# Kernel optimization log

Measured on AMD Instinct MI355X. Metric: run time of the kernel, lower is better.

Reference implementation:

```python
import jax, jax.numpy as jnp
import numpy as np

N = 100000        # nodes
E = 1600000       # edges
D = 128           # feature dim (all layers)
G = 128           # graphs
C = 10            # num_classes
L = 3             # conv layers
EPS = 1e-5
SLOPE = 0.03


def setup_inputs() -> dict:
    key = jax.random.key(0)
    ks = jax.random.split(key, 12)
    x = jax.random.normal(ks[0], (N, D), dtype=jnp.float32)
    edge_index = jax.random.randint(ks[1], (2, E), 0, N, dtype=jnp.int64)
    batch = jnp.sort(jax.random.randint(ks[2], (N,), 0, G, dtype=jnp.int64))
    s = 1.0 / np.sqrt(D)
    Wc = jax.random.uniform(ks[3], (L, D, D), jnp.float32, -s, s)
    bc = jax.random.uniform(ks[4], (L, D), jnp.float32, -s, s)
    bn_gamma = jnp.ones((2, D), jnp.float32)
    bn_beta = jnp.zeros((2, D), jnp.float32)
    bn_mean = jax.random.normal(ks[5], (2, D), jnp.float32) * 0.1
    bn_var = jax.random.uniform(ks[6], (2, D), jnp.float32, 0.5, 1.5)
    lin_w = jax.random.uniform(ks[7], (C, D), jnp.float32, -s, s)
    lin_b = jax.random.uniform(ks[8], (C,), jnp.float32, -s, s)
    return {"x": x, "edge_index": edge_index, "batch": batch, "Wc": Wc,
            "bc": bc, "bn_gamma": bn_gamma, "bn_beta": bn_beta,
            "bn_mean": bn_mean, "bn_var": bn_var, "lin_w": lin_w, "lin_b": lin_b}


def _gcn_norm(edge_index):
    # add self-loops, compute D^{-1/2}[row] * D^{-1/2}[col] (PyG gcn_norm)
    loops = jnp.arange(N, dtype=edge_index.dtype)
    row = jnp.concatenate([edge_index[0], loops])
    col = jnp.concatenate([edge_index[1], loops])
    deg = jax.ops.segment_sum(jnp.ones_like(col, dtype=jnp.float32), col, num_segments=N)
    dis = jnp.where(deg > 0, jax.lax.rsqrt(deg), 0.0)
    return row, col, dis[row] * dis[col]


def reference(x, edge_index, batch, Wc, bc, bn_gamma, bn_beta, bn_mean, bn_var, lin_w, lin_b):
    row, col, norm = _gcn_norm(edge_index)
    h = x
    for i in range(L):
        h = h @ Wc[i]                                          # linear transform [N, D]
        msg = h[row] * norm[:, None]                           # gather + normalize [E+N, D]
        h = jax.ops.segment_sum(msg, col, num_segments=N) + bc[i]
        if i < 2:  # batchnorm only for i < len(batchnorms)-1 (eval mode, running stats)
            h = (h - bn_mean[i]) * jax.lax.rsqrt(bn_var[i] + EPS) * bn_gamma[i] + bn_beta[i]
        h = jnp.where(h > 0, h, SLOPE * h)                     # LeakyReLU(0.03)
    # global mean pool over graphs
    counts = jax.ops.segment_sum(jnp.ones((N,), jnp.float32), batch, num_segments=G)
    pooled = jax.ops.segment_sum(h, batch, num_segments=G) / jnp.maximum(counts, 1.0)[:, None]
    # dropout is identity in eval; final linear head
    return pooled @ lin_w.T + lin_b                            # [G, C]
```

## Files before the change

kernel.cpp:

```cpp
#include <hip/hip_runtime.h>
#include <hip/hip_bf16.h>

#define NN 100000
#define EE 1600000
#define DD 128
#define GG 128
#define CC 10
#define NPB 256
#define NB 391
#define SCAP 5120
#define VPT 16
#define CPAD 32
#define PPN 64

typedef __attribute__((ext_vector_type(8))) short bf16x8;
typedef __attribute__((ext_vector_type(4))) float f32x4;
typedef __attribute__((ext_vector_type(2))) float f32x2;
typedef unsigned int u32;

__device__ inline float blo(u32 u) { return __uint_as_float(u << 16); }
__device__ inline float bhi(u32 u) { return __uint_as_float(u & 0xffff0000u); }
__device__ inline u32 bpack(float x, float y) {
    u32 bx = __float_as_uint(x);
    u32 by = __float_as_uint(y);
    bx = (bx + 0x7fffu + ((bx >> 16) & 1u)) >> 16;
    by = (by + 0x7fffu + ((by >> 16) & 1u)) & 0xffff0000u;
    return bx | by;
}

__global__ __launch_bounds__(256) void k_bcount(const int* __restrict__ col,
                                                int* __restrict__ bhist) {
    __shared__ int lh[NB];
    int tid = threadIdx.x;
    for (int b = tid; b < NB; b += 256) lh[b] = 0;
    __syncthreads();
    int base = blockIdx.x * (256 * VPT);
#pragma unroll
    for (int j = 0; j < VPT; j++) {
        int e = base + j * 256 + tid;
        if (e < EE) atomicAdd(&lh[col[e] >> 8], 1);
    }
    __syncthreads();
    for (int b = tid; b < NB; b += 256) {
        int h = lh[b];
        if (h) atomicAdd(&bhist[b * CPAD], h);
    }
}

__global__ __launch_bounds__(512) void k_bscan(const int* __restrict__ bhist,
                                               int* __restrict__ boffs,
                                               int* __restrict__ bcur) {
    __shared__ int s[512];
    int tid = threadIdx.x;
    int c = (tid < NB) ? bhist[tid * CPAD] : 0;
    s[tid] = c;
    __syncthreads();
    for (int off = 1; off < 512; off <<= 1) {
        int v = (tid >= off) ? s[tid - off] : 0;
        __syncthreads();
        s[tid] += v;
        __syncthreads();
    }
    int excl = s[tid] - c;
    if (tid < NB) {
        boffs[tid] = excl;
        bcur[tid * CPAD] = excl;
    }
    if (tid == NB - 1) boffs[NB] = excl + c;
}

__global__ __launch_bounds__(256) void k_part(const int* __restrict__ row, const int* __restrict__ col,
                                              int* __restrict__ bcur, u32* __restrict__ pairs) {
    __shared__ int lhist[NB];
    __shared__ int gbase[NB];
    __shared__ int lcur[NB];
    int tid = threadIdx.x;
    for (int b = tid; b < NB; b += 256) lhist[b] = 0;
    __syncthreads();
    int base = blockIdx.x * (256 * VPT);
    u32 v[VPT];
    int bb[VPT];
#pragma unroll
    for (int j = 0; j < VPT; j++) {
        int e = base + j * 256 + tid;
        if (e < EE) {
            int r = row[e], c = col[e];
            v[j] = ((u32)r << 8) | (u32)(c & 255);
            bb[j] = c >> 8;
            atomicAdd(&lhist[bb[j]], 1);
        } else {
            bb[j] = -1;
        }
    }
    __syncthreads();
    for (int b = tid; b < NB; b += 256) {
        int h = lhist[b];
        gbase[b] = h ? atomicAdd(&bcur[b * CPAD], h) : 0;
        lcur[b] = 0;
    }
    __syncthreads();
#pragma unroll
    for (int j = 0; j < VPT; j++) {
        if (bb[j] >= 0) {
            int slot = gbase[bb[j]] + atomicAdd(&lcur[bb[j]], 1);
            pairs[slot] = v[j];
        }
    }
}

__global__ __launch_bounds__(256) void k_sort(const u32* __restrict__ pairs,
                                              const int* __restrict__ boffs,
                                              int* __restrict__ offs,
                                              float* __restrict__ dis,
                                              int* __restrict__ src) {
    int b = blockIdx.x;
    int tid = threadIdx.x;
    int nstart = b << 8;
    int nvalid = NN - nstart;
    if (nvalid > NPB) nvalid = NPB;
    int base = boffs[b];
    int eend = boffs[b + 1];
    int cnt = eend - base;
    __shared__ int lcnt[NPB];
    __shared__ int lscan[NPB];
    __shared__ int lcur[NPB];
    __shared__ int lsrc[SCAP];
    lcnt[tid] = 0;
    __syncthreads();
    for (int e = base + tid; e < eend; e += 256)
        atomicAdd(&lcnt[pairs[e] & 255u], 1);
    __syncthreads();
    int c = lcnt[tid];
    lscan[tid] = c;
    __syncthreads();
    for (int off = 1; off < 256; off <<= 1) {
        int v = (tid >= off) ? lscan[tid - off] : 0;
        __syncthreads();
        lscan[tid] += v;
        __syncthreads();
    }
    int excl = lscan[tid] - c;
    if (tid < nvalid) {
        offs[nstart + tid] = base + excl;
        dis[nstart + tid] = rsqrtf((float)(c + 1));
    }
    if (b == NB - 1 && tid == 255) offs[NN] = EE;
    lcur[tid] = excl;
    __syncthreads();
    if (cnt <= SCAP) {
        for (int e = base + tid; e < eend; e += 256) {
            u32 v = pairs[e];
            int slot = atomicAdd(&lcur[v & 255u], 1);
            lsrc[slot] = (int)(v >> 8);
        }
        __syncthreads();
        for (int i = tid; i < cnt; i += 256)
            src[base + i] = lsrc[i];
    } else {
        for (int e = base + tid; e < eend; e += 256) {
            u32 v = pairs[e];
            int slot = base + atomicAdd(&lcur[v & 255u], 1);
            src[slot] = (int)(v >> 8);
        }
    }
}

__global__ void k_prep(const float* __restrict__ Wc, const float* __restrict__ bc,
                       const float* __restrict__ gamma, const float* __restrict__ beta,
                       const float* __restrict__ mean, const float* __restrict__ var,
                       __hip_bfloat16* __restrict__ WT,
                       float* __restrict__ tc) {
    int i = blockIdx.x * 256 + threadIdx.x;
    if (i < 3 * 128) {
        int l = i >> 7, d = i & 127;
        float t;
        if (l < 2) {
            float s = gamma[l * 128 + d] * rsqrtf(var[l * 128 + d] + 1e-5f);
            t = (bc[l * 128 + d] - mean[l * 128 + d]) * s + beta[l * 128 + d];
        } else {
            t = bc[2 * 128 + d];
        }
        tc[i] = t;
    }
    if (i < 3 * 16384) {
        int l = i >> 14, r = (i >> 7) & 127, k = i & 127;
        float s = 1.f;
        if (l < 2) s = gamma[l * 128 + r] * rsqrtf(var[l * 128 + r] + 1e-5f);
        WT[i] = __float2bfloat16(Wc[l * 16384 + k * 128 + r] * s);
    }
}

__global__ __launch_bounds__(256) void k_pre(const float* __restrict__ x,
                                             const float* __restrict__ dis,
                                             u32* __restrict__ hs) {
    int i = blockIdx.x * 256 + threadIdx.x;
    if (i < NN * 64) {
        float dn = dis[i >> 6];
        float2 v = ((const float2*)x)[i];
        hs[i] = bpack(v.x * dn, v.y * dn);
    }
}

template <int PRESCALE>
__global__ __launch_bounds__(1024) void k_aggT(const u32* __restrict__ hin,
                                               const int* __restrict__ offs,
                                               const int* __restrict__ src,
                                               const float* __restrict__ dis,
                                               const __hip_bfloat16* __restrict__ WT,
                                               const float* __restrict__ tc,
                                               u32* __restrict__ hout) {
    __shared__ u32   Atile[16][68];
    __shared__ float Otile[16][132];
    int wid = threadIdx.x >> 6;
    int lane = threadIdx.x & 63;
    int node = blockIdx.x * 16 + wid;
    int e0 = __builtin_amdgcn_readfirstlane(offs[node]);
    int e1 = __builtin_amdgcn_readfirstlane(offs[node + 1]);
    u32 self = hin[((u32)node << 6) + lane];
    f32x2 acc = {blo(self), bhi(self)};
    int e = e0;
    for (; e + 16 <= e1; e += 16) {
        u32 u[16];
#pragma unroll
        for (int j = 0; j < 16; j++) {
            u32 s = (u32)src[e + j];
            u[j] = hin[(s << 6) + lane];
        }
#pragma unroll
        for (int j = 0; j < 16; j++) {
            f32x2 v = {blo(u[j]), bhi(u[j])};
            acc += v;
        }
    }
    for (; e + 8 <= e1; e += 8) {
        u32 u[8];
#pragma unroll
        for (int j = 0; j < 8; j++) {
            u32 s = (u32)src[e + j];
            u[j] = hin[(s << 6) + lane];
        }
#pragma unroll
        for (int j = 0; j < 8; j++) {
            f32x2 v = {blo(u[j]), bhi(u[j])};
            acc += v;
        }
    }
    for (; e < e1; e++) {
        u32 u = hin[((u32)src[e] << 6) + lane];
        f32x2 v = {blo(u), bhi(u)};
        acc += v;
    }
    float dn = dis[node];
    Atile[wid][lane] = bpack(acc.x * dn, acc.y * dn);
    __syncthreads();
    if (wid < 8) {
        int lg = lane >> 4, lr = lane & 15;
        f32x4 c4 = {0.f, 0.f, 0.f, 0.f};
#pragma unroll
        for (int kk = 0; kk < 4; kk++) {
            bf16x8 a = *(const bf16x8*)&Atile[lr][kk * 16 + lg * 4];
            bf16x8 b = *(const bf16x8*)(WT + (size_t)(wid * 16 + lr) * 128 + kk * 32 + lg * 8);
            c4 = __builtin_amdgcn_mfma_f32_16x16x32_bf16(a, b, c4, 0, 0, 0);
        }
#pragma unroll
        for (int r = 0; r < 4; r++)
            Otile[lg * 4 + r][wid * 16 + lr] = c4[r];
    }
    __syncthreads();
    int d0 = lane * 2;
    float r0 = Otile[wid][d0]     + tc[d0];
    float r1 = Otile[wid][d0 + 1] + tc[d0 + 1];
    r0 = r0 > 0.f ? r0 : 0.03f * r0;
    r1 = r1 > 0.f ? r1 : 0.03f * r1;
    if (PRESCALE) { r0 *= dn; r1 *= dn; }
    hout[((u32)node << 6) + lane] = bpack(r0, r1);
}

__global__ __launch_bounds__(64) void k_pool(const u32* __restrict__ h,
                                             const int* __restrict__ batch,
                                             float* __restrict__ pooled,
                                             float* __restrict__ counts) {
    int lane = threadIdx.x;
    int n0 = blockIdx.x * PPN;
    if (n0 >= NN) return;
    int n1 = n0 + PPN;
    if (n1 > NN) n1 = NN;
    float a0 = 0.f, a1 = 0.f, cnt = 0.f;
    int g = batch[n0];
    for (int n = n0; n < n1; n++) {
        int bg = batch[n];
        if (bg != g) {
            atomicAdd(&pooled[g * 128 + lane * 2], a0);
            atomicAdd(&pooled[g * 128 + lane * 2 + 1], a1);
            if (lane == 0) atomicAdd(&counts[g], cnt);
            a0 = 0.f; a1 = 0.f; cnt = 0.f; g = bg;
        }
        u32 u = h[(u32)n * 64u + lane];
        a0 += blo(u); a1 += bhi(u);
        cnt += 1.f;
    }
    atomicAdd(&pooled[g * 128 + lane * 2], a0);
    atomicAdd(&pooled[g * 128 + lane * 2 + 1], a1);
    if (lane == 0) atomicAdd(&counts[g], cnt);
}

__global__ void k_head(const float* __restrict__ pooled, const float* __restrict__ counts,
                       const float* __restrict__ w, const float* __restrict__ b,
                       float* __restrict__ out) {
    int i = blockIdx.x * blockDim.x + threadIdx.x;
    if (i >= GG * CC) return;
    int g = i / CC, c = i % CC;
    float cnt = counts[g];
    cnt = cnt > 1.f ? cnt : 1.f;
    float inv = 1.f / cnt;
    const float* p = &pooled[g * 128];
    const float* ww = &w[c * 128];
    float acc = 0.f;
    for (int d = 0; d < 128; d++) acc += p[d] * ww[d];
    out[i] = acc * inv + b[c];
}

extern "C" void kernel_launch(void* const* d_in, const int* in_sizes, int n_in,
                              void* d_out, int out_size, void* d_ws, size_t ws_size,
                              hipStream_t stream) {
    const float* x     = (const float*)d_in[0];
    const int*   ei    = (const int*)d_in[1];
    const int*   row   = ei;
    const int*   col   = ei + EE;
    const int*   batch = (const int*)d_in[2];
    const float* Wc    = (const float*)d_in[3];
    const float* bc    = (const float*)d_in[4];
    const float* gamma = (const float*)d_in[5];
    const float* beta  = (const float*)d_in[6];
    const float* mean  = (const float*)d_in[7];
    const float* var   = (const float*)d_in[8];
    const float* lw    = (const float*)d_in[9];
    const float* lb    = (const float*)d_in[10];
    float* out = (float*)d_out;

    char* p = (char*)d_ws;
    auto alloc = [&](size_t bytes) -> char* {
        char* r = p;
        p += (bytes + 255) & ~(size_t)255;
        return r;
    };
    float* dis    = (float*)alloc((size_t)NN * 4);
    int*   offs   = (int*)alloc((size_t)(NN + 1) * 4);
    int*   bhist  = (int*)alloc((size_t)NB * CPAD * 4);
    int*   boffs  = (int*)alloc((size_t)(NB + 1) * 4);
    int*   bcur   = (int*)alloc((size_t)NB * CPAD * 4);
    int*   src    = (int*)alloc((size_t)EE * 4);
    __hip_bfloat16* WT = (__hip_bfloat16*)alloc((size_t)3 * 16384 * 2);
    float* tc     = (float*)alloc((size_t)3 * 128 * 4);
    float* pooled = (float*)alloc((size_t)GG * 128 * 4);
    float* counts = (float*)alloc((size_t)GG * 4);
    __hip_bfloat16* h0b = (__hip_bfloat16*)alloc((size_t)NN * 128 * 2);
    __hip_bfloat16* h1b = (__hip_bfloat16*)alloc((size_t)NN * 128 * 2);
    u32* pairs = (u32*)h0b;

    hipMemsetAsync(bhist, 0, (size_t)NB * CPAD * 4, stream);
    hipMemsetAsync(pooled, 0, (size_t)GG * 128 * 4, stream);
    hipMemsetAsync(counts, 0, (size_t)GG * 4, stream);

    const int eb_grid = (EE + 256 * VPT - 1) / (256 * VPT);
    k_bcount<<<eb_grid, 256, 0, stream>>>(col, bhist);
    k_bscan<<<1, 512, 0, stream>>>(bhist, boffs, bcur);
    k_part<<<eb_grid, 256, 0, stream>>>(row, col, bcur, pairs);
    k_sort<<<NB, 256, 0, stream>>>(pairs, boffs, offs, dis, src);
    k_prep<<<192, 256, 0, stream>>>(Wc, bc, gamma, beta, mean, var, WT, tc);
    k_pre<<<(NN * 64 + 255) / 256, 256, 0, stream>>>(x, dis, (u32*)h0b);

    const int fused_grid = NN / 16;

    k_aggT<1><<<fused_grid, 1024, 0, stream>>>((const u32*)h0b, offs, src, dis, WT,           tc,       (u32*)h1b);
    k_aggT<1><<<fused_grid, 1024, 0, stream>>>((const u32*)h1b, offs, src, dis, WT + 16384,   tc + 128, (u32*)h0b);
    k_aggT<0><<<fused_grid, 1024, 0, stream>>>((const u32*)h0b, offs, src, dis, WT + 2*16384, tc + 256, (u32*)h1b);

    k_pool<<<(NN + PPN - 1) / PPN, 64, 0, stream>>>((const u32*)h1b, batch, pooled, counts);
    k_head<<<(GG * CC + 255) / 256, 256, 0, stream>>>(pooled, counts, lw, lb, out);
}
```

Baseline: 379.9 us.

## Sort nodes by in-degree so each aggregation block handles similar-degree nodes

Adds a counting sort of nodes by in-degree (histogram, scan, fill kernels) that builds a permutation. Each wave of the fused aggregate+transform kernel then processes permuted nodes, so the 16 waves in a block have similar edge counts. The aim is to reduce load imbalance and idle waves that wait at block barriers. In exchange it adds three small kernels and an extra indirection, and it scatters output writes and self reads, which loses the locality of sequential node order.

```diff
diff --git a/kernel.cpp b/kernel.cpp
--- a/kernel.cpp
+++ b/kernel.cpp
@@ -12,6 +12,7 @@
 #define VPT 16
 #define CPAD 32
 #define PPN 64
+#define DB 256
 
 typedef __attribute__((ext_vector_type(8))) short bf16x8;
 typedef __attribute__((ext_vector_type(4))) float f32x4;
@@ -112,6 +113,7 @@
                                               const int* __restrict__ boffs,
                                               int* __restrict__ offs,
                                               float* __restrict__ dis,
+                                              int* __restrict__ deg,
                                               int* __restrict__ src) {
     int b = blockIdx.x;
     int tid = threadIdx.x;
@@ -143,6 +145,7 @@
     if (tid < nvalid) {
         offs[nstart + tid] = base + excl;
         dis[nstart + tid] = rsqrtf((float)(c + 1));
+        deg[nstart + tid] = c;
     }
     if (b == NB - 1 && tid == 255) offs[NN] = EE;
     lcur[tid] = excl;
@@ -161,6 +164,75 @@
             u32 v = pairs[e];
             int slot = base + atomicAdd(&lcur[v & 255u], 1);
             src[slot] = (int)(v >> 8);
+        }
+    }
+}
+
+__global__ __launch_bounds__(256) void k_dhist(const int* __restrict__ deg,
+                                               int* __restrict__ dh) {
+    __shared__ int lh[DB];
+    int tid = threadIdx.x;
+    lh[tid] = 0;
+    __syncthreads();
+    int base = blockIdx.x * 1024;
+#pragma unroll
+    for (int j = 0; j < 4; j++) {
+        int n = base + j * 256 + tid;
+        if (n < NN) {
+            int d = deg[n]; if (d > 255) d = 255;
+            atomicAdd(&lh[d], 1);
+        }
+    }
+    __syncthreads();
+    int h = lh[tid];
+    if (h) atomicAdd(&dh[tid * CPAD], h);
+}
+
+__global__ __launch_bounds__(256) void k_dscan(const int* __restrict__ dh,
+                                               int* __restrict__ dcur) {
+    __shared__ int s[DB];
+    int tid = threadIdx.x;
+    int c = dh[tid * CPAD];
+    s[tid] = c;
+    __syncthreads();
+    for (int off = 1; off < DB; off <<= 1) {
+        int v = (tid >= off) ? s[tid - off] : 0;
+        __syncthreads();
+        s[tid] += v;
+        __syncthreads();
+    }
+    dcur[tid * CPAD] = s[tid] - c;
+}
+
+__global__ __launch_bounds__(256) void k_dfill(const int* __restrict__ deg,
+                                               int* __restrict__ dcur,
+                                               int* __restrict__ perm) {
+    __shared__ int lh[DB];
+    __shared__ int gb[DB];
+    __shared__ int lc[DB];
+    int tid = threadIdx.x;
+    lh[tid] = 0;
+    __syncthreads();
+    int base = blockIdx.x * 1024;
+    int d[4];
+#pragma unroll
+    for (int j = 0; j < 4; j++) {
+        int n = base + j * 256 + tid;
+        if (n < NN) {
+            d[j] = deg[n]; if (d[j] > 255) d[j] = 255;
+            atomicAdd(&lh[d[j]], 1);
+        } else d[j] = -1;
+    }
+    __syncthreads();
+    int h = lh[tid];
+    gb[tid] = h ? atomicAdd(&dcur[tid * CPAD], h) : 0;
+    lc[tid] = 0;
+    __syncthreads();
+#pragma unroll
+    for (int j = 0; j < 4; j++) {
+        if (d[j] >= 0) {
+            int r = atomicAdd(&lc[d[j]], 1);
+            perm[gb[d[j]] + r] = base + j * 256 + tid;
         }
     }
 }
@@ -206,6 +278,7 @@
                                                const int* __restrict__ offs,
                                                const int* __restrict__ src,
                                                const float* __restrict__ dis,
+                                               const int* __restrict__ perm,
                                                const __hip_bfloat16* __restrict__ WT,
                                                const float* __restrict__ tc,
                                                u32* __restrict__ hout) {
@@ -213,7 +286,7 @@
     __shared__ float Otile[16][132];
     int wid = threadIdx.x >> 6;
     int lane = threadIdx.x & 63;
-    int node = blockIdx.x * 16 + wid;
+    int node = __builtin_amdgcn_readfirstlane(perm[blockIdx.x * 16 + wid]);
     int e0 = __builtin_amdgcn_readfirstlane(offs[node]);
     int e1 = __builtin_amdgcn_readfirstlane(offs[node + 1]);
     u32 self = hin[((u32)node << 6) + lane];
@@ -346,9 +419,13 @@
     };
     float* dis    = (float*)alloc((size_t)NN * 4);
     int*   offs   = (int*)alloc((size_t)(NN + 1) * 4);
+    int*   deg    = (int*)alloc((size_t)NN * 4);
+    int*   perm   = (int*)alloc((size_t)NN * 4);
     int*   bhist  = (int*)alloc((size_t)NB * CPAD * 4);
     int*   boffs  = (int*)alloc((size_t)(NB + 1) * 4);
     int*   bcur   = (int*)alloc((size_t)NB * CPAD * 4);
+    int*   dh     = (int*)alloc((size_t)DB * CPAD * 4);
+    int*   dcur   = (int*)alloc((size_t)DB * CPAD * 4);
     int*   src    = (int*)alloc((size_t)EE * 4);
     __hip_bfloat16* WT = (__hip_bfloat16*)alloc((size_t)3 * 16384 * 2);
     float* tc     = (float*)alloc((size_t)3 * 128 * 4);
@@ -359,22 +436,27 @@
     u32* pairs = (u32*)h0b;
 
     hipMemsetAsync(bhist, 0, (size_t)NB * CPAD * 4, stream);
+    hipMemsetAsync(dh, 0, (size_t)DB * CPAD * 4, stream);
     hipMemsetAsync(pooled, 0, (size_t)GG * 128 * 4, stream);
     hipMemsetAsync(counts, 0, (size_t)GG * 4, stream);
 
     const int eb_grid = (EE + 256 * VPT - 1) / (256 * VPT);
+    const int nd_grid = (NN + 1023) / 1024;
     k_bcount<<<eb_grid, 256, 0, stream>>>(col, bhist);
     k_bscan<<<1, 512, 0, stream>>>(bhist, boffs, bcur);
     k_part<<<eb_grid, 256, 0, stream>>>(row, col, bcur, pairs);
-    k_sort<<<NB, 256, 0, stream>>>(pairs, boffs, offs, dis, src);
+    k_sort<<<NB, 256, 0, stream>>>(pairs, boffs, offs, dis, deg, src);
+    k_dhist<<<nd_grid, 256, 0, stream>>>(deg, dh);
+    k_dscan<<<1, 256, 0, stream>>>(dh, dcur);
+    k_dfill<<<nd_grid, 256, 0, stream>>>(deg, dcur, perm);
     k_prep<<<192, 256, 0, stream>>>(Wc, bc, gamma, beta, mean, var, WT, tc);
     k_pre<<<(NN * 64 + 255) / 256, 256, 0, stream>>>(x, dis, (u32*)h0b);
 
     const int fused_grid = NN / 16;
 
-    k_aggT<1><<<fused_grid, 1024, 0, stream>>>((const u32*)h0b, offs, src, dis, WT,           tc,       (u32*)h1b);
-    k_aggT<1><<<fused_grid, 1024, 0, stream>>>((const u32*)h1b, offs, src, dis, WT + 16384,   tc + 128, (u32*)h0b);
-    k_aggT<0><<<fused_grid, 1024, 0, stream>>>((const u32*)h0b, offs, src, dis, WT + 2*16384, tc + 256, (u32*)h1b);
+    k_aggT<1><<<fused_grid, 1024, 0, stream>>>((const u32*)h0b, offs, src, dis, perm, WT,           tc,       (u32*)h1b);
+    k_aggT<1><<<fused_grid, 1024, 0, stream>>>((const u32*)h1b, offs, src, dis, perm, WT + 16384,   tc + 128, (u32*)h0b);
+    k_aggT<0><<<fused_grid, 1024, 0, stream>>>((const u32*)h0b, offs, src, dis, perm, WT + 2*16384, tc + 256, (u32*)h1b);
 
     k_pool<<<(NN + PPN - 1) / PPN, 64, 0, stream>>>((const u32*)h1b, batch, pooled, counts);
     k_head<<<(GG * CC + 255) / 256, 256, 0, stream>>>(pooled, counts, lw, lb, out);
```

Result: faster. 370.5 us (-2.5%).

## Split fused aggregate+transform kernel into separate gather and MFMA transform kernels

Applied to the files above, without the earlier changes.

Replaces the fused 1024-thread kernel, which did the neighbour gather and then an MFMA transform in one block, with two kernels per layer. A 256-thread gather kernel writes the aggregated bf16 rows to memory, and a separate 512-thread kernel applies the 128x128 MFMA transform, bias and LeakyReLU in place. The aim is to drop the block-wide syncs and large blocks that stall gather waves, and to let small blocks schedule flexibly for better latency hiding. The cost is an extra round trip of the node features through global memory and three extra launches.

```diff
diff --git a/kernel.cpp b/kernel.cpp
--- a/kernel.cpp
+++ b/kernel.cpp
@@ -201,19 +201,14 @@
     }
 }
 
-template <int PRESCALE>
-__global__ __launch_bounds__(1024) void k_aggT(const u32* __restrict__ hin,
-                                               const int* __restrict__ offs,
-                                               const int* __restrict__ src,
-                                               const float* __restrict__ dis,
-                                               const __hip_bfloat16* __restrict__ WT,
-                                               const float* __restrict__ tc,
-                                               u32* __restrict__ hout) {
-    __shared__ u32   Atile[16][68];
-    __shared__ float Otile[16][132];
-    int wid = threadIdx.x >> 6;
+__global__ __launch_bounds__(256) void k_agg2(const u32* __restrict__ hin,
+                                              const int* __restrict__ offs,
+                                              const int* __restrict__ src,
+                                              const float* __restrict__ dis,
+                                              u32* __restrict__ aggout) {
+    int node = (blockIdx.x << 2) + (threadIdx.x >> 6);
     int lane = threadIdx.x & 63;
-    int node = blockIdx.x * 16 + wid;
+    if (node >= NN) return;
     int e0 = __builtin_amdgcn_readfirstlane(offs[node]);
     int e1 = __builtin_amdgcn_readfirstlane(offs[node + 1]);
     u32 self = hin[((u32)node << 6) + lane];
@@ -251,29 +246,45 @@
         acc += v;
     }
     float dn = dis[node];
-    Atile[wid][lane] = bpack(acc.x * dn, acc.y * dn);
-    __syncthreads();
-    if (wid < 8) {
-        int lg = lane >> 4, lr = lane & 15;
-        f32x4 c4 = {0.f, 0.f, 0.f, 0.f};
-#pragma unroll
-        for (int kk = 0; kk < 4; kk++) {
-            bf16x8 a = *(const bf16x8*)&Atile[lr][kk * 16 + lg * 4];
-            bf16x8 b = *(const bf16x8*)(WT + (size_t)(wid * 16 + lr) * 128 + kk * 32 + lg * 8);
-            c4 = __builtin_amdgcn_mfma_f32_16x16x32_bf16(a, b, c4, 0, 0, 0);
-        }
-#pragma unroll
-        for (int r = 0; r < 4; r++)
-            Otile[lg * 4 + r][wid * 16 + lr] = c4[r];
-    }
-    __syncthreads();
-    int d0 = lane * 2;
-    float r0 = Otile[wid][d0]     + tc[d0];
-    float r1 = Otile[wid][d0 + 1] + tc[d0 + 1];
-    r0 = r0 > 0.f ? r0 : 0.03f * r0;
-    r1 = r1 > 0.f ? r1 : 0.03f * r1;
-    if (PRESCALE) { r0 *= dn; r1 *= dn; }
-    hout[((u32)node << 6) + lane] = bpack(r0, r1);
+    aggout[((u32)node << 6) + lane] = bpack(acc.x * dn, acc.y * dn);
+}
+
+template <int PRESCALE>
+__global__ __launch_bounds__(512) void k_trans(u32* __restrict__ h,
+                                               const float* __restrict__ dis,
+                                               const __hip_bfloat16* __restrict__ WT,
+                                               const float* __restrict__ tc) {
+    __shared__ u32   Atile[16][68];
+    __shared__ float Otile[16][132];
+    int tid = threadIdx.x;
+    int row0 = blockIdx.x * 16;
+    for (int i = tid; i < 1024; i += 512)
+        Atile[i >> 6][i & 63] = h[(u32)row0 * 64u + i];
+    __syncthreads();
+    int wid = tid >> 6, lane = tid & 63;
+    int lg = lane >> 4, lr = lane & 15;
+    f32x4 c4 = {0.f, 0.f, 0.f, 0.f};
+#pragma unroll
+    for (int kk = 0; kk < 4; kk++) {
+        bf16x8 a = *(const bf16x8*)&Atile[lr][kk * 16 + lg * 4];
+        bf16x8 b = *(const bf16x8*)(WT + (size_t)(wid * 16 + lr) * 128 + kk * 32 + lg * 8);
+        c4 = __builtin_amdgcn_mfma_f32_16x16x32_bf16(a, b, c4, 0, 0, 0);
+    }
+#pragma unroll
+    for (int r = 0; r < 4; r++)
+        Otile[lg * 4 + r][wid * 16 + lr] = c4[r];
+    __syncthreads();
+    for (int i = tid; i < 1024; i += 512) {
+        int rw = i >> 6, cp = i & 63;
+        int node = row0 + rw;
+        int d0 = cp * 2;
+        float r0 = Otile[rw][d0]     + tc[d0];
+        float r1 = Otile[rw][d0 + 1] + tc[d0 + 1];
+        r0 = r0 > 0.f ? r0 : 0.03f * r0;
+        r1 = r1 > 0.f ? r1 : 0.03f * r1;
+        if (PRESCALE) { float dn = dis[node]; r0 *= dn; r1 *= dn; }
+        h[(u32)node * 64u + cp] = bpack(r0, r1);
+    }
 }
 
 __global__ __launch_bounds__(64) void k_pool(const u32* __restrict__ h,
@@ -370,11 +381,15 @@
     k_prep<<<192, 256, 0, stream>>>(Wc, bc, gamma, beta, mean, var, WT, tc);
     k_pre<<<(NN * 64 + 255) / 256, 256, 0, stream>>>(x, dis, (u32*)h0b);
 
-    const int fused_grid = NN / 16;
-
-    k_aggT<1><<<fused_grid, 1024, 0, stream>>>((const u32*)h0b, offs, src, dis, WT,           tc,       (u32*)h1b);
-    k_aggT<1><<<fused_grid, 1024, 0, stream>>>((const u32*)h1b, offs, src, dis, WT + 16384,   tc + 128, (u32*)h0b);
-    k_aggT<0><<<fused_grid, 1024, 0, stream>>>((const u32*)h0b, offs, src, dis, WT + 2*16384, tc + 256, (u32*)h1b);
+    const int agg_grid   = NN / 4;
+    const int trans_grid = NN / 16;
+
+    k_agg2<<<agg_grid, 256, 0, stream>>>((const u32*)h0b, offs, src, dis, (u32*)h1b);
+    k_trans<1><<<trans_grid, 512, 0, stream>>>((u32*)h1b, dis, WT, tc);
+    k_agg2<<<agg_grid, 256, 0, stream>>>((const u32*)h1b, offs, src, dis, (u32*)h0b);
+    k_trans<1><<<trans_grid, 512, 0, stream>>>((u32*)h0b, dis, WT + 16384, tc + 128);
+    k_agg2<<<agg_grid, 256, 0, stream>>>((const u32*)h0b, offs, src, dis, (u32*)h1b);
+    k_trans<0><<<trans_grid, 512, 0, stream>>>((u32*)h1b, dis, WT + 2 * 16384, tc + 256);
 
     k_pool<<<(NN + PPN - 1) / PPN, 64, 0, stream>>>((const u32*)h1b, batch, pooled, counts);
     k_head<<<(GG * CC + 255) / 256, 256, 0, stream>>>(pooled, counts, lw, lb, out);
```

After: 387.9 us. 1.02x slower.

## Make each wave aggregate eight nodes and run its own MFMA transform

Applied to the files above, without the earlier changes.

The fused aggregate-plus-transform kernel now has each 64-lane wave gather eight nodes serially, then compute all eight output column tiles with MFMA from its own LDS tile. This removes the block-wide __syncthreads barriers and the idle waves in the old layout, where 16 waves each handled one node and only 8 of them ran MFMA. In exchange, each wave's gather latency is serialized across its eight nodes. Half of each MFMA's A rows are duplicates and are wasted, and blocks shrink to 256 threads.

```diff
diff --git a/kernel.cpp b/kernel.cpp
--- a/kernel.cpp
+++ b/kernel.cpp
@@ -202,78 +202,89 @@
 }
 
 template <int PRESCALE>
-__global__ __launch_bounds__(1024) void k_aggT(const u32* __restrict__ hin,
-                                               const int* __restrict__ offs,
-                                               const int* __restrict__ src,
-                                               const float* __restrict__ dis,
-                                               const __hip_bfloat16* __restrict__ WT,
-                                               const float* __restrict__ tc,
-                                               u32* __restrict__ hout) {
-    __shared__ u32   Atile[16][68];
-    __shared__ float Otile[16][132];
-    int wid = threadIdx.x >> 6;
-    int lane = threadIdx.x & 63;
-    int node = blockIdx.x * 16 + wid;
-    int e0 = __builtin_amdgcn_readfirstlane(offs[node]);
-    int e1 = __builtin_amdgcn_readfirstlane(offs[node + 1]);
-    u32 self = hin[((u32)node << 6) + lane];
-    f32x2 acc = {blo(self), bhi(self)};
-    int e = e0;
-    for (; e + 16 <= e1; e += 16) {
-        u32 u[16];
-#pragma unroll
-        for (int j = 0; j < 16; j++) {
-            u32 s = (u32)src[e + j];
-            u[j] = hin[(s << 6) + lane];
-        }
-#pragma unroll
-        for (int j = 0; j < 16; j++) {
-            f32x2 v = {blo(u[j]), bhi(u[j])};
+__global__ __launch_bounds__(256) void k_aggW(const u32* __restrict__ hin,
+                                              const int* __restrict__ offs,
+                                              const int* __restrict__ src,
+                                              const float* __restrict__ dis,
+                                              const __hip_bfloat16* __restrict__ WT,
+                                              const float* __restrict__ tc,
+                                              u32* __restrict__ hout) {
+    __shared__ u32   Atile[4][8][68];
+    __shared__ float Otile[4][8][132];
+    int tid = threadIdx.x;
+    int w = tid >> 6, lane = tid & 63;
+    int base = blockIdx.x * 32 + w * 8;
+    float dns[8];
+#pragma unroll
+    for (int i = 0; i < 8; i++) {
+        int node = base + i;
+        int e0 = __builtin_amdgcn_readfirstlane(offs[node]);
+        int e1 = __builtin_amdgcn_readfirstlane(offs[node + 1]);
+        u32 self = hin[((u32)node << 6) + lane];
+        f32x2 acc = {blo(self), bhi(self)};
+        int e = e0;
+        for (; e + 16 <= e1; e += 16) {
+            u32 u[16];
+#pragma unroll
+            for (int j = 0; j < 16; j++) {
+                u32 s = (u32)src[e + j];
+                u[j] = hin[(s << 6) + lane];
+            }
+#pragma unroll
+            for (int j = 0; j < 16; j++) {
+                f32x2 v = {blo(u[j]), bhi(u[j])};
+                acc += v;
+            }
+        }
+        for (; e + 8 <= e1; e += 8) {
+            u32 u[8];
+#pragma unroll
+            for (int j = 0; j < 8; j++) {
+                u32 s = (u32)src[e + j];
+                u[j] = hin[(s << 6) + lane];
+            }
+#pragma unroll
+            for (int j = 0; j < 8; j++) {
+                f32x2 v = {blo(u[j]), bhi(u[j])};
+                acc += v;
+            }
+        }
+        for (; e < e1; e++) {
+            u32 u = hin[((u32)src[e] << 6) + lane];
+            f32x2 v = {blo(u), bhi(u)};
             acc += v;
         }
-    }
-    for (; e + 8 <= e1; e += 8) {
-        u32 u[8];
-#pragma unroll
-        for (int j = 0; j < 8; j++) {
-            u32 s = (u32)src[e + j];
-            u[j] = hin[(s << 6) + lane];
-        }
-#pragma unroll
-        for (int j = 0; j < 8; j++) {
-            f32x2 v = {blo(u[j]), bhi(u[j])};
-            acc += v;
-        }
-    }
-    for (; e < e1; e++) {
-        u32 u = hin[((u32)src[e] << 6) + lane];
-        f32x2 v = {blo(u), bhi(u)};
-        acc += v;
-    }
-    float dn = dis[node];
-    Atile[wid][lane] = bpack(acc.x * dn, acc.y * dn);
-    __syncthreads();
-    if (wid < 8) {
-        int lg = lane >> 4, lr = lane & 15;
+        float dn = dis[node];
+        dns[i] = dn;
+        Atile[w][i][lane] = bpack(acc.x * dn, acc.y * dn);
+    }
+    int lg = lane >> 4, lr = lane & 15;
+#pragma unroll
+    for (int ct = 0; ct < 8; ct++) {
         f32x4 c4 = {0.f, 0.f, 0.f, 0.f};
 #pragma unroll
         for (int kk = 0; kk < 4; kk++) {
-            bf16x8 a = *(const bf16x8*)&Atile[lr][kk * 16 + lg * 4];
-            bf16x8 b = *(const bf16x8*)(WT + (size_t)(wid * 16 + lr) * 128 + kk * 32 + lg * 8);
+            bf16x8 a = *(const bf16x8*)&Atile[w][lr & 7][kk * 16 + lg * 4];
+            bf16x8 b = *(const bf16x8*)(WT + (size_t)(ct * 16 + lr) * 128 + kk * 32 + lg * 8);
             c4 = __builtin_amdgcn_mfma_f32_16x16x32_bf16(a, b, c4, 0, 0, 0);
         }
-#pragma unroll
-        for (int r = 0; r < 4; r++)
-            Otile[lg * 4 + r][wid * 16 + lr] = c4[r];
-    }
-    __syncthreads();
+        if (lg < 2) {
+#pragma unroll
+            for (int r = 0; r < 4; r++)
+                Otile[w][lg * 4 + r][ct * 16 + lr] = c4[r];
+        }
+    }
     int d0 = lane * 2;
-    float r0 = Otile[wid][d0]     + tc[d0];
-    float r1 = Otile[wid][d0 + 1] + tc[d0 + 1];
-    r0 = r0 > 0.f ? r0 : 0.03f * r0;
-    r1 = r1 > 0.f ? r1 : 0.03f * r1;
-    if (PRESCALE) { r0 *= dn; r1 *= dn; }
-    hout[((u32)node << 6) + lane] = bpack(r0, r1);
+    float t0 = tc[d0], t1 = tc[d0 + 1];
+#pragma unroll
+    for (int i = 0; i < 8; i++) {
+        float r0 = Otile[w][i][d0]     + t0;
+        float r1 = Otile[w][i][d0 + 1] + t1;
+        r0 = r0 > 0.f ? r0 : 0.03f * r0;
+        r1 = r1 > 0.f ? r1 : 0.03f * r1;
+        if (PRESCALE) { r0 *= dns[i]; r1 *= dns[i]; }
+        hout[((u32)(base + i) << 6) + lane] = bpack(r0, r1);
+    }
 }
 
 __global__ __launch_bounds__(64) void k_pool(const u32* __restrict__ h,
@@ -370,11 +381,11 @@
     k_prep<<<192, 256, 0, stream>>>(Wc, bc, gamma, beta, mean, var, WT, tc);
     k_pre<<<(NN * 64 + 255) / 256, 256, 0, stream>>>(x, dis, (u32*)h0b);
 
-    const int fused_grid = NN / 16;
-
-    k_aggT<1><<<fused_grid, 1024, 0, stream>>>((const u32*)h0b, offs, src, dis, WT,           tc,       (u32*)h1b);
-    k_aggT<1><<<fused_grid, 1024, 0, stream>>>((const u32*)h1b, offs, src, dis, WT + 16384,   tc + 128, (u32*)h0b);
-    k_aggT<0><<<fused_grid, 1024, 0, stream>>>((const u32*)h0b, offs, src, dis, WT + 2*16384, tc + 256, (u32*)h1b);
+    const int fused_grid = NN / 32;
+
+    k_aggW<1><<<fused_grid, 256, 0, stream>>>((const u32*)h0b, offs, src, dis, WT,           tc,       (u32*)h1b);
+    k_aggW<1><<<fused_grid, 256, 0, stream>>>((const u32*)h1b, offs, src, dis, WT + 16384,   tc + 128, (u32*)h0b);
+    k_aggW<0><<<fused_grid, 256, 0, stream>>>((const u32*)h0b, offs, src, dis, WT + 2*16384, tc + 256, (u32*)h1b);
 
     k_pool<<<(NN + PPN - 1) / PPN, 64, 0, stream>>>((const u32*)h1b, batch, pooled, counts);
     k_head<<<(GG * CC + 255) / 256, 256, 0, stream>>>(pooled, counts, lw, lb, out);
```

Result: slower. 436.0 us (+14.8%).
